# Performance work log

Hardware: AMD Instinct MI355X
Metric: run time of the kernel (lower is better)

Reference implementation:

```python
import jax, jax.numpy as jnp
from jax import lax
import numpy as np
from functools import partial

B, N, T, H, L = 16, 256, 4, 128, 2
VOCAB, OUT_VOCAB, MAX_STEPS = 1000, 1000, 15


def setup_inputs() -> dict:
    key = jax.random.key(0)
    ks = jax.random.split(key, 13)
    data = jax.random.randint(ks[0], (B, N, T), 0, VOCAB)
    true_branch_nodes = jax.random.randint(ks[1], (B, N), 0, N)
    false_branch_nodes = jax.random.randint(ks[2], (B, N), 0, N)
    exit_index = jax.random.randint(ks[3], (B,), 0, N)
    steps = jax.random.randint(ks[4], (B,), 1, MAX_STEPS + 1)
    s_in = 1.0 / np.sqrt(H)
    s_cat = 1.0 / np.sqrt(2 * L * H)
    embed = jax.random.uniform(ks[5], (VOCAB, H), jnp.float32, -0.1, 0.1)
    Wi = jax.random.normal(ks[6], (L, H, 4 * H), jnp.float32) * s_in
    Wh = jax.random.normal(ks[7], (L, H, 4 * H), jnp.float32) * s_in
    b_lstm = jnp.zeros((L, 4 * H), jnp.float32)
    Wb = jax.random.normal(ks[8], (2 * L * H, 2), jnp.float32) * s_cat
    bb = jax.random.normal(ks[9], (2,), jnp.float32) * 1e-6
    Wo = jax.random.normal(ks[10], (2 * L * H, OUT_VOCAB), jnp.float32) * s_cat
    bo = jax.random.normal(ks[11], (OUT_VOCAB,), jnp.float32) * 1e-6
    return dict(data=data, true_branch_nodes=true_branch_nodes,
                false_branch_nodes=false_branch_nodes, exit_index=exit_index,
                steps=steps, embed=embed, Wi=Wi, Wh=Wh, b_lstm=b_lstm,
                Wb=Wb, bb=bb, Wo=Wo, bo=bo)


def _lstm_step(Wi_l, Wh_l, b_l, c, h, x):
    # flax LSTMCell math: gates from input (no bias) + recurrent (bias)
    z = x @ Wi_l + h @ Wh_l + b_l  # [..., 4H]
    i, f, g, o = jnp.split(z, 4, axis=-1)
    c2 = jax.nn.sigmoid(f) * c + jax.nn.sigmoid(i) * jnp.tanh(g)
    h2 = jax.nn.sigmoid(o) * jnp.tanh(c2)
    return c2, h2


def _forward(data, true_branch_nodes, false_branch_nodes, exit_index, steps,
             embed, Wi, Wh, b_lstm, Wb, bb, Wo, bo):
    emb = embed[data]                       # [B, N, T, H]
    cs = jnp.zeros((L, B, N, H), embed.dtype)
    hs = jnp.zeros((L, B, N, H), embed.dtype)
    ip = jnp.zeros((B, N), embed.dtype).at[:, 0].set(1.0)
    b_idx = jnp.arange(B)

    seg_b = jax.vmap(partial(jax.ops.segment_sum, num_segments=N))        # [B,N,...] , [B,N]
    seg_lb = jax.vmap(seg_b, in_axes=(0, None))                           # [L,B,N,H]

    def execute(cs, hs):
        # run the stacked LSTM over the T statement tokens at every node
        def tok_step(carry, x_t):
            cs, hs = carry
            inp = x_t
            nc, nh = [], []
            for l in range(L):
                c2, h2 = _lstm_step(Wi[l], Wh[l], b_lstm[l], cs[l], hs[l], inp)
                nc.append(c2); nh.append(h2)
                inp = h2
            return (jnp.stack(nc), jnp.stack(nh)), None
        (cs, hs), _ = lax.scan(tok_step, (cs, hs), jnp.moveaxis(emb, 2, 0))
        return cs, hs

    def step(carry, _):
        cs, hs, ip, idx = carry
        cs_c, hs_c = execute(cs, hs)
        # exit node keeps its previous hidden state
        cs_c = cs_c.at[:, b_idx, exit_index].set(cs[:, b_idx, exit_index])
        hs_c = hs_c.at[:, b_idx, exit_index].set(hs[:, b_idx, exit_index])
        # branch decision from concatenated (c, h) of every layer: [B, N, 2LH]
        feats = jnp.concatenate([x for l in range(L) for x in (cs_c[l], hs_c[l])], axis=-1)
        branch = jax.nn.softmax(feats @ Wb + bb, axis=-1)
        wt = branch[..., 0] * ip            # [B, N]
        wf = branch[..., 1] * ip
        ip_new = seg_b(wt, true_branch_nodes) + seg_b(wf, false_branch_nodes)
        denom = (ip_new + 1e-7)[None, :, :, None]
        def agg(h):
            return (seg_lb(h * wt[None, :, :, None], true_branch_nodes)
                    + seg_lb(h * wf[None, :, :, None], false_branch_nodes)) / denom
        cs_new, hs_new = agg(cs_c), agg(hs_c)
        live = idx < steps                   # [B]
        cs = jnp.where(live[None, :, None, None], cs_new, cs)
        hs = jnp.where(live[None, :, None, None], hs_new, hs)
        ip = jnp.where(live[:, None], ip_new, ip)
        return (cs, hs, ip, idx + 1), None

    (cs, hs, ip, _), _ = lax.scan(step, (cs, hs, ip, jnp.zeros((), jnp.int32)),
                                  None, length=MAX_STEPS)
    fc = cs[:, b_idx, exit_index]           # [L, B, H]
    fh = hs[:, b_idx, exit_index]
    final = jnp.concatenate([x for l in range(L) for x in (fc[l], fh[l])], axis=-1)
    logits = final @ Wo + bo                # [B, OUT_VOCAB]
    return logits[:, None, :]


def reference(data, true_branch_nodes, false_branch_nodes, exit_index, steps,
              embed, Wi, Wh, b_lstm, Wb, bb, Wo, bo):
    return _forward(data, true_branch_nodes, false_branch_nodes, exit_index,
                    steps, embed, Wi, Wh, b_lstm, Wb, bb, Wo, bo)
```

## Files before the change

### kernel.cpp

```cpp
#include <hip/hip_runtime.h>
#include <hip/hip_bf16.h>
#include <stdint.h>
#include <stddef.h>

static constexpr int BB = 16, NN = 256, TT = 4, HH = 128;
static constexpr int MM = BB * NN;
static constexpr int CC = 512;
static constexpr int OUTV = 1000;
static constexpr int MAXS = 15;
static constexpr int SP = 132;

typedef float f32x4 __attribute__((ext_vector_type(4)));
typedef short s16x8 __attribute__((ext_vector_type(8)));

__device__ __forceinline__ float sigf(float x) { return 1.0f / (1.0f + __expf(-x)); }
__device__ __forceinline__ float tanhr(float x) { return 2.0f / (1.0f + __expf(-2.0f * x)) - 1.0f; }
__device__ __forceinline__ unsigned short f2bu(float a) {
  return __builtin_bit_cast(unsigned short, __float2bfloat16(a));
}
__device__ __forceinline__ unsigned int packh(float a, float b) {
  return (unsigned int)f2bu(a) | ((unsigned int)f2bu(b) << 16);
}
__device__ __forceinline__ float blo(unsigned int u) { return __builtin_bit_cast(float, u << 16); }
__device__ __forceinline__ float bhi(unsigned int u) { return __builtin_bit_cast(float, u & 0xffff0000u); }


__global__ __launch_bounds__(512) void csr_kernel(const int* __restrict__ tb,
                                                  const int* __restrict__ fb,
                                                  int* __restrict__ offs,
                                                  int* __restrict__ edges) {
  const int blk = blockIdx.x;
  const int tid = threadIdx.x;
  __shared__ int cnt[256], sc[256], cur[256];
  if (tid < 256) cnt[tid] = 0;
  __syncthreads();
  const int n = tid >> 1, bit = tid & 1;
  const int tgt = bit ? fb[blk * NN + n] : tb[blk * NN + n];
  atomicAdd(&cnt[tgt], 1);
  __syncthreads();
  if (tid < 256) sc[tid] = cnt[tid];
  __syncthreads();
  for (int ofs = 1; ofs < 256; ofs <<= 1) {
    int t2 = (tid < 256 && tid >= ofs) ? sc[tid - ofs] : 0;
    __syncthreads();
    if (tid < 256) sc[tid] += t2;
    __syncthreads();
  }
  if (tid < 256) { offs[blk * NN + tid] = blk * 2 * NN + sc[tid] - cnt[tid]; cur[tid] = 0; }
  if (blk == 0 && tid == 0) offs[MM] = 2 * MM;
  __syncthreads();
  int lpos = sc[tgt] - cnt[tgt] + atomicAdd(&cur[tgt], 1);
  edges[blk * 2 * NN + lpos] = (n << 1) | bit;
}

__global__ __launch_bounds__(256) void prep_kernel(
    const float* __restrict__ Wh0, const float* __restrict__ Wi1, const float* __restrict__ Wh1,
    const float* __restrict__ embed, const float* __restrict__ Wi0, const float* __restrict__ b0,
    unsigned short* __restrict__ swz, float* __restrict__ tab) {
  const int blk = blockIdx.x;
  const int tid = threadIdx.x;
  if (blk < 768) {
    int i = blk * 256 + tid;
    int mtx = i >> 16, ii = i & 65535;
    const float* W = (mtx == 0) ? Wh0 : (mtx == 1) ? Wi1 : Wh1;
    int j = ii & 7, ln = (ii >> 3) & 63, kb = (ii >> 9) & 3, ct = ii >> 11;
    int n = ln & 15, q = ln >> 4;
    swz[i] = f2bu(W[(kb * 32 + q * 8 + j) * CC + ct * 16 + n]);
    return;
  }
  const int v0 = (blk - 768) * 8;
  __shared__ float A[8][HH];
  for (int s = tid; s < 8 * HH; s += 256) {
    int r = s >> 7, k = s & 127;
    A[r][k] = embed[(size_t)(v0 + r) * HH + k];
  }
  __syncthreads();
  const int j = tid;
  float za[8], zb[8];
  {
    float ba = b0[j], bbv = b0[j + 256];
#pragma unroll
    for (int r = 0; r < 8; ++r) { za[r] = ba; zb[r] = bbv; }
  }
#pragma unroll 4
  for (int k = 0; k < HH; ++k) {
    float wa = Wi0[k * CC + j], wb = Wi0[k * CC + j + 256];
#pragma unroll
    for (int r = 0; r < 8; ++r) { za[r] += A[r][k] * wa; zb[r] += A[r][k] * wb; }
  }
#pragma unroll
  for (int r = 0; r < 8; ++r) {
    tab[(size_t)(v0 + r) * CC + j] = za[r];
    tab[(size_t)(v0 + r) * CC + j + 256] = zb[r];
  }
}


__global__ __launch_bounds__(512) void step_kernel(
    float* __restrict__ Sc0g, float* __restrict__ Sh0g,
    float* __restrict__ Sc1g, float* __restrict__ Sh1g,
    const unsigned int* __restrict__ Pr, unsigned int* __restrict__ Pw,
    const float* __restrict__ wtR, const float* __restrict__ wfR,
    float* __restrict__ wtW, float* __restrict__ wfW,
    const int* __restrict__ offs, const int* __restrict__ edges,
    const float* __restrict__ tab,
    const unsigned short* __restrict__ swzWh0, const unsigned short* __restrict__ swzWi1,
    const unsigned short* __restrict__ swzWh1, const float* __restrict__ b1,
    const float* __restrict__ Wb, const float* __restrict__ bb,
    const int* __restrict__ data, const int* __restrict__ exi,
    const int* __restrict__ steps, int step) {
  const int B = blockIdx.x;
  const int b = (B & 7) | (((B >> 3) & 1) << 3);
  const int g16 = B >> 4;
  const int row0 = b * NN + g16 * 16;
  const int sb = steps[b];
  const bool aggLive = (step >= 1) && ((step - 1) < sb);
  const bool lstmLive = (step < sb);
  if (!aggLive && !lstmLive) return;

  const int tid = threadIdx.x;
  const int w = tid >> 6;
  const int lane = tid & 63;
  const int n16 = lane & 15, qq = lane >> 4;
  const int kcol = w * 16 + n16;
  const int basePos = ((kcol >> 5) * 64 + ((kcol >> 3) & 3) * 16) * 8 + (kcol & 7);

  __shared__ float c0L[16 * SP], h0L[16 * SP], c1L[16 * SP], h1L[16 * SP];
  __shared__ __align__(16) unsigned short hA0[2][2048], hA1[2][2048];
  __shared__ float exitP[512];
  __shared__ float ipL[16];
  __shared__ int toks[64];

  s16x8 B0f[4][4], B1f[4][4];
  float b1v[4];
  const s16x8* pWh0 = (const s16x8*)swzWh0;
  const s16x8* pWh1 = (const s16x8*)swzWh1;
  const s16x8* pWi1 = (const s16x8*)swzWi1;
  if (lstmLive) {
#pragma unroll
    for (int g = 0; g < 4; ++g) {
      int ci = w + 8 * g;
#pragma unroll
      for (int kb = 0; kb < 4; ++kb) {
        B0f[g][kb] = pWh0[(ci * 4 + kb) * 64 + lane];
        B1f[g][kb] = pWh1[(ci * 4 + kb) * 64 + lane];
      }
      b1v[g] = b1[ci * 16 + n16];
    }
    if (tid < 64) toks[tid] = data[(row0 + (tid >> 2)) * TT + (tid & 3)];
  }

  if (aggLive) {
    const int l = tid & 31;
    const int m = tid >> 5;
    const int node = row0 + m;
    const int beg = offs[node], end = offs[node + 1];
    float ac0[4] = {0,0,0,0}, ah0[4] = {0,0,0,0}, ac1[4] = {0,0,0,0}, ah1[4] = {0,0,0,0};
    float wsum = 0.f;
    for (int e = beg; e < end; ++e) {
      int rec = edges[e];
      int src = (b << 8) + (rec >> 1);
      float wv = (rec & 1) ? wfR[src] : wtR[src];
      wsum += wv;
      const uint4* pr = (const uint4*)(Pr + (size_t)src * 256 + 8 * l);
      uint4 u0 = pr[0], u1 = pr[1];
      ac0[0] += wv * blo(u0.x); ac0[1] += wv * bhi(u0.x);
      ac0[2] += wv * blo(u0.y); ac0[3] += wv * bhi(u0.y);
      ah0[0] += wv * blo(u0.z); ah0[1] += wv * bhi(u0.z);
      ah0[2] += wv * blo(u0.w); ah0[3] += wv * bhi(u0.w);
      ac1[0] += wv * blo(u1.x); ac1[1] += wv * bhi(u1.x);
      ac1[2] += wv * blo(u1.y); ac1[3] += wv * bhi(u1.y);
      ah1[0] += wv * blo(u1.z); ah1[1] += wv * bhi(u1.z);
      ah1[2] += wv * blo(u1.w); ah1[3] += wv * bhi(u1.w);
    }
    float inv = 1.0f / (wsum + 1e-7f);
    float4 o0 = { ac0[0]*inv, ac0[1]*inv, ac0[2]*inv, ac0[3]*inv };
    float4 o1 = { ah0[0]*inv, ah0[1]*inv, ah0[2]*inv, ah0[3]*inv };
    float4 o2 = { ac1[0]*inv, ac1[1]*inv, ac1[2]*inv, ac1[3]*inv };
    float4 o3 = { ah1[0]*inv, ah1[1]*inv, ah1[2]*inv, ah1[3]*inv };
    ((float4*)c0L)[m * (SP / 4) + l] = o0;
    ((float4*)h0L)[m * (SP / 4) + l] = o1;
    ((float4*)c1L)[m * (SP / 4) + l] = o2;
    ((float4*)h1L)[m * (SP / 4) + l] = o3;
    if (l == 0) ipL[m] = wsum;
    if (!lstmLive) {
      ((float4*)Sc0g)[node * 32 + l] = o0;
      ((float4*)Sh0g)[node * 32 + l] = o1;
      ((float4*)Sc1g)[node * 32 + l] = o2;
      ((float4*)Sh1g)[node * 32 + l] = o3;
    }
  } else {
    for (int i2 = tid; i2 < 16 * HH; i2 += 512) {
      int m = i2 >> 7, k = i2 & 127;
      c0L[m * SP + k] = 0.f; h0L[m * SP + k] = 0.f;
      c1L[m * SP + k] = 0.f; h1L[m * SP + k] = 0.f;
    }
    if (tid < 16) ipL[tid] = (((row0 + tid) & (NN - 1)) == 0) ? 1.0f : 0.0f;
  }
  if (!lstmLive) return;

  const int exnode = exi[b];
  const int exm = exnode - (g16 * 16);
  __syncthreads();

  if (exm >= 0 && exm < 16 && tid < 128) {
    exitP[tid] = c0L[exm * SP + tid];
    exitP[128 + tid] = h0L[exm * SP + tid];
    exitP[256 + tid] = c1L[exm * SP + tid];
    exitP[384 + tid] = h1L[exm * SP + tid];
  }

  float c0r[4], c1r[4], h0r[4], h1r[4];
#pragma unroll
  for (int r = 0; r < 4; ++r) {
    int m = qq * 4 + r;
    c0r[r] = c0L[m * SP + kcol];
    c1r[r] = c1L[m * SP + kcol];
    h0r[r] = h0L[m * SP + kcol];
    h1r[r] = h1L[m * SP + kcol];
    hA0[0][basePos + m * 8] = f2bu(h0r[r]);
    hA1[0][basePos + m * 8] = f2bu(h1r[r]);
  }
  __syncthreads();

  int cur = 0;
  for (int t = 0; t < TT; ++t) {
    const int nxt = cur ^ 1;
    const s16x8* hA0c = (const s16x8*)hA0[cur];
    const s16x8* hA1c = (const s16x8*)hA1[cur];
    s16x8 a0[4], a1b[4];
#pragma unroll
    for (int kb = 0; kb < 4; ++kb) { a0[kb] = hA0c[kb * 64 + lane]; a1b[kb] = hA1c[kb * 64 + lane]; }
    f32x4 d0[4];
#pragma unroll
    for (int g = 0; g < 4; ++g) {
      int colz = (w + 8 * g) * 16 + n16;
#pragma unroll
      for (int r = 0; r < 4; ++r)
        d0[g][r] = tab[(size_t)toks[(qq * 4 + r) * 4 + t] * CC + colz];
    }

#pragma unroll
    for (int g = 0; g < 4; ++g)
#pragma unroll
      for (int kb = 0; kb < 4; ++kb)
        d0[g] = __builtin_amdgcn_mfma_f32_16x16x32_bf16(a0[kb], B0f[g][kb], d0[g], 0, 0, 0);

#pragma unroll
    for (int r = 0; r < 4; ++r) {
      float cn = sigf(d0[1][r]) * c0r[r] + sigf(d0[0][r]) * tanhr(d0[2][r]);
      float hn = sigf(d0[3][r]) * tanhr(cn);
      c0r[r] = cn; h0r[r] = hn;
      hA0[nxt][basePos + (qq * 4 + r) * 8] = f2bu(hn);
    }
    __syncthreads();

    const s16x8* hA0n = (const s16x8*)hA0[nxt];
    s16x8 a1a[4];
#pragma unroll
    for (int kb = 0; kb < 4; ++kb) a1a[kb] = hA0n[kb * 64 + lane];
    f32x4 d1[4];
#pragma unroll
    for (int g = 0; g < 4; ++g) {
      int ci = w + 8 * g;
      s16x8 wi[4];
#pragma unroll
      for (int kb = 0; kb < 4; ++kb) wi[kb] = pWi1[(ci * 4 + kb) * 64 + lane];
      f32x4 d = { b1v[g], b1v[g], b1v[g], b1v[g] };
#pragma unroll
      for (int kb = 0; kb < 4; ++kb)
        d = __builtin_amdgcn_mfma_f32_16x16x32_bf16(a1a[kb], wi[kb], d, 0, 0, 0);
#pragma unroll
      for (int kb = 0; kb < 4; ++kb)
        d = __builtin_amdgcn_mfma_f32_16x16x32_bf16(a1b[kb], B1f[g][kb], d, 0, 0, 0);
      d1[g] = d;
    }

#pragma unroll
    for (int r = 0; r < 4; ++r) {
      float cn = sigf(d1[1][r]) * c1r[r] + sigf(d1[0][r]) * tanhr(d1[2][r]);
      float hn = sigf(d1[3][r]) * tanhr(cn);
      c1r[r] = cn; h1r[r] = hn;
      hA1[nxt][basePos + (qq * 4 + r) * 8] = f2bu(hn);
    }
    __syncthreads();
    cur = nxt;
  }

#pragma unroll
  for (int r = 0; r < 4; ++r) {
    int m = qq * 4 + r;
    c0L[m * SP + kcol] = c0r[r];
    h0L[m * SP + kcol] = h0r[r];
    c1L[m * SP + kcol] = c1r[r];
    h1L[m * SP + kcol] = h1r[r];
  }
  __syncthreads();

  {
    const int m = tid >> 5, sub = tid & 31;
    const int row = row0 + m;
    const bool isExit = (m == exm);
    float z0 = 0.f, z1 = 0.f;
#pragma unroll
    for (int u = 0; u < 16; ++u) {
      int k = u * 32 + sub;
      int seg = k >> 7, kk = k & 127;
      float fk;
      if (isExit) {
        fk = exitP[seg * 128 + kk];
      } else {
        fk = (seg == 0) ? c0L[m * SP + kk] : (seg == 1) ? h0L[m * SP + kk]
           : (seg == 2) ? c1L[m * SP + kk] : h1L[m * SP + kk];
      }
      z0 += fk * Wb[2 * k];
      z1 += fk * Wb[2 * k + 1];
    }
#pragma unroll
    for (int off = 16; off >= 1; off >>= 1) {
      z0 += __shfl_xor(z0, off);
      z1 += __shfl_xor(z1, off);
    }
    if (sub == 0) {
      z0 += bb[0]; z1 += bb[1];
      float mx = fmaxf(z0, z1);
      float e0 = __expf(z0 - mx), e1 = __expf(z1 - mx);
      float inv = 1.0f / (e0 + e1);
      float ipv = ipL[m];
      wtW[row] = e0 * inv * ipv;
      wfW[row] = e1 * inv * ipv;
    }
  }

  {
    const int m = tid >> 5, l = tid & 31;
    const bool ex = (m == exm);
    const int grow = row0 + m;
    float f0[4], f1[4], f2[4], f3[4];
#pragma unroll
    for (int i = 0; i < 4; ++i) {
      int k = 4 * l + i;
      f0[i] = ex ? exitP[k] : c0L[m * SP + k];
      f1[i] = ex ? exitP[128 + k] : h0L[m * SP + k];
      f2[i] = ex ? exitP[256 + k] : c1L[m * SP + k];
      f3[i] = ex ? exitP[384 + k] : h1L[m * SP + k];
    }
    uint4 o0 = { packh(f0[0], f0[1]), packh(f0[2], f0[3]),
                 packh(f1[0], f1[1]), packh(f1[2], f1[3]) };
    uint4 o1 = { packh(f2[0], f2[1]), packh(f2[2], f2[3]),
                 packh(f3[0], f3[1]), packh(f3[2], f3[3]) };
    uint4* pw = (uint4*)(Pw + (size_t)grow * 256 + 8 * l);
    pw[0] = o0; pw[1] = o1;
  }
}

__global__ void final_kernel(const float* __restrict__ Sc0, const float* __restrict__ Sh0,
                             const float* __restrict__ Sc1, const float* __restrict__ Sh1,
                             const int* __restrict__ exi, const float* __restrict__ Wo,
                             const float* __restrict__ bo, float* __restrict__ out) {
  const int b = blockIdx.x >> 2;
  const int vt = blockIdx.x & 3;
  const int tid = threadIdx.x;
  __shared__ float f[512];
  int row = b * NN + exi[b];
  if (tid < 128) {
    size_t g = (size_t)row * HH + tid;
    f[tid] = Sc0[g];
    f[128 + tid] = Sh0[g];
    f[256 + tid] = Sc1[g];
    f[384 + tid] = Sh1[g];
  }
  __syncthreads();
  if (tid < 250) {
    int v = vt * 250 + tid;
    float acc = bo[v];
#pragma unroll 8
    for (int k = 0; k < 512; ++k) acc += f[k] * Wo[(size_t)k * OUTV + v];
    out[b * OUTV + v] = acc;
  }
}

__global__ void zero_out_kernel(float* __restrict__ out, int n) {
  int i = blockIdx.x * blockDim.x + threadIdx.x;
  if (i < n) out[i] = 0.0f;
}


extern "C" void kernel_launch(void* const* d_in, const int* in_sizes, int n_in,
                              void* d_out, int out_size, void* d_ws, size_t ws_size,
                              hipStream_t stream) {
  const int* data = (const int*)d_in[0];
  const int* tb   = (const int*)d_in[1];
  const int* fb   = (const int*)d_in[2];
  const int* exi  = (const int*)d_in[3];
  const int* steps = (const int*)d_in[4];
  const float* embed = (const float*)d_in[5];
  const float* Wi = (const float*)d_in[6];
  const float* Wh = (const float*)d_in[7];
  const float* bl = (const float*)d_in[8];
  const float* Wb = (const float*)d_in[9];
  const float* bb = (const float*)d_in[10];
  const float* Wo = (const float*)d_in[11];
  const float* bo = (const float*)d_in[12];
  float* out = (float*)d_out;

  const float* Wi0 = Wi;
  const float* Wi1 = Wi + HH * CC;
  const float* Wh0 = Wh;
  const float* Wh1 = Wh + HH * CC;
  const float* b0 = bl;
  const float* b1 = bl + CC;

  float* ws = (float*)d_ws;
  size_t off = 0;
  float* tab = ws + off;  off += (size_t)1024 * CC;
  float* Sc0 = ws + off;  off += (size_t)MM * HH;
  float* Sh0 = ws + off;  off += (size_t)MM * HH;
  float* Sc1 = ws + off;  off += (size_t)MM * HH;
  float* Sh1 = ws + off;  off += (size_t)MM * HH;
  unsigned int* PA = (unsigned int*)(ws + off); off += (size_t)MM * 256;
  unsigned int* PB = (unsigned int*)(ws + off); off += (size_t)MM * 256;
  unsigned short* swz = (unsigned short*)(ws + off); off += 3 * 32768;
  float* wtA = ws + off;  off += MM;
  float* wfA = ws + off;  off += MM;
  float* wtB = ws + off;  off += MM;
  float* wfB = ws + off;  off += MM;
  int* offs  = (int*)(ws + off); off += MM + 16;
  int* edges = (int*)(ws + off); off += 2 * MM;
  (void)in_sizes; (void)n_in; (void)out_size;

  if (ws_size < off * sizeof(float)) {
    zero_out_kernel<<<(BB * OUTV + 255) / 256, 256, 0, stream>>>(out, BB * OUTV);
    return;
  }

  unsigned short* swzWh0 = swz;
  unsigned short* swzWi1 = swz + 65536;
  unsigned short* swzWh1 = swz + 2 * 65536;

  csr_kernel<<<BB, 512, 0, stream>>>(tb, fb, offs, edges);
  prep_kernel<<<893, 256, 0, stream>>>(Wh0, Wi1, Wh1, embed, Wi0, b0, swz, tab);

  for (int s = 0; s <= MAXS; ++s) {
    unsigned int* Pwp = (s & 1) ? PB : PA;
    const unsigned int* Prp = (s & 1) ? PA : PB;
    float* wtWp = (s & 1) ? wtB : wtA;
    float* wfWp = (s & 1) ? wfB : wfA;
    const float* wtRp = (s & 1) ? wtA : wtB;
    const float* wfRp = (s & 1) ? wfA : wfB;
    step_kernel<<<MM / 16, 512, 0, stream>>>(
        Sc0, Sh0, Sc1, Sh1, Prp, Pwp,
        wtRp, wfRp, wtWp, wfWp,
        offs, edges, tab, swzWh0, swzWi1, swzWh1, b1, Wb, bb,
        data, exi, steps, s);
  }
  final_kernel<<<BB * 4, 256, 0, stream>>>(Sc0, Sh0, Sc1, Sh1, exi, Wo, bo, out);
}
```

Before: 551.1 us.

## Fuse setup kernels, fold final projection into step kernel, prefetch next token gates

Merges the CSR build and weight-prep kernels into one launch, with the prep tiles resized to 512 threads. The output projection now runs inside the step kernel: when a batch finishes aggregating, only the block that owns the exit node computes the logits directly, so the four full-state global buffers and the final kernel are removed. The per-token embedding-gate table loads are prefetched one timestep ahead so they overlap the layer-1 MFMA work. Risks are fewer blocks doing the logits (each computes 1000 outputs over 512 inputs), plus extra register pressure from the prefetch buffers.

```diff
diff --git a/kernel.cpp b/kernel.cpp
--- a/kernel.cpp
+++ b/kernel.cpp
@@ -24,43 +24,41 @@
 __device__ __forceinline__ float blo(unsigned int u) { return __builtin_bit_cast(float, u << 16); }
 __device__ __forceinline__ float bhi(unsigned int u) { return __builtin_bit_cast(float, u & 0xffff0000u); }
 
-
-__global__ __launch_bounds__(512) void csr_kernel(const int* __restrict__ tb,
-                                                  const int* __restrict__ fb,
-                                                  int* __restrict__ offs,
-                                                  int* __restrict__ edges) {
-  const int blk = blockIdx.x;
-  const int tid = threadIdx.x;
-  __shared__ int cnt[256], sc[256], cur[256];
-  if (tid < 256) cnt[tid] = 0;
-  __syncthreads();
-  const int n = tid >> 1, bit = tid & 1;
-  const int tgt = bit ? fb[blk * NN + n] : tb[blk * NN + n];
-  atomicAdd(&cnt[tgt], 1);
-  __syncthreads();
-  if (tid < 256) sc[tid] = cnt[tid];
-  __syncthreads();
-  for (int ofs = 1; ofs < 256; ofs <<= 1) {
-    int t2 = (tid < 256 && tid >= ofs) ? sc[tid - ofs] : 0;
-    __syncthreads();
-    if (tid < 256) sc[tid] += t2;
-    __syncthreads();
-  }
-  if (tid < 256) { offs[blk * NN + tid] = blk * 2 * NN + sc[tid] - cnt[tid]; cur[tid] = 0; }
-  if (blk == 0 && tid == 0) offs[MM] = 2 * MM;
-  __syncthreads();
-  int lpos = sc[tgt] - cnt[tgt] + atomicAdd(&cur[tgt], 1);
-  edges[blk * 2 * NN + lpos] = (n << 1) | bit;
-}
-
-__global__ __launch_bounds__(256) void prep_kernel(
+__global__ __launch_bounds__(512) void setup_kernel(
+    const int* __restrict__ tb, const int* __restrict__ fb,
+    int* __restrict__ offs, int* __restrict__ edges,
     const float* __restrict__ Wh0, const float* __restrict__ Wi1, const float* __restrict__ Wh1,
     const float* __restrict__ embed, const float* __restrict__ Wi0, const float* __restrict__ b0,
     unsigned short* __restrict__ swz, float* __restrict__ tab) {
   const int blk = blockIdx.x;
   const int tid = threadIdx.x;
-  if (blk < 768) {
-    int i = blk * 256 + tid;
+  __shared__ int cnt[256], sc[256], cur[256];
+  __shared__ float A[8][HH];
+
+  if (blk < 16) {
+    if (tid < 256) cnt[tid] = 0;
+    __syncthreads();
+    const int n = tid >> 1, bit = tid & 1;
+    const int tgt = bit ? fb[blk * NN + n] : tb[blk * NN + n];
+    atomicAdd(&cnt[tgt], 1);
+    __syncthreads();
+    if (tid < 256) sc[tid] = cnt[tid];
+    __syncthreads();
+    for (int ofs = 1; ofs < 256; ofs <<= 1) {
+      int t2 = (tid < 256 && tid >= ofs) ? sc[tid - ofs] : 0;
+      __syncthreads();
+      if (tid < 256) sc[tid] += t2;
+      __syncthreads();
+    }
+    if (tid < 256) { offs[blk * NN + tid] = blk * 2 * NN + sc[tid] - cnt[tid]; cur[tid] = 0; }
+    if (blk == 0 && tid == 0) offs[MM] = 2 * MM;
+    __syncthreads();
+    int lpos = sc[tgt] - cnt[tgt] + atomicAdd(&cur[tgt], 1);
+    edges[blk * 2 * NN + lpos] = (n << 1) | bit;
+    return;
+  }
+  if (blk < 400) {
+    int i = (blk - 16) * 512 + tid;
     int mtx = i >> 16, ii = i & 65535;
     const float* W = (mtx == 0) ? Wh0 : (mtx == 1) ? Wi1 : Wh1;
     int j = ii & 7, ln = (ii >> 3) & 63, kb = (ii >> 9) & 3, ct = ii >> 11;
@@ -68,37 +66,31 @@
     swz[i] = f2bu(W[(kb * 32 + q * 8 + j) * CC + ct * 16 + n]);
     return;
   }
-  const int v0 = (blk - 768) * 8;
-  __shared__ float A[8][HH];
-  for (int s = tid; s < 8 * HH; s += 256) {
+  const int v0 = (blk - 400) * 8;
+  for (int s = tid; s < 8 * HH; s += 512) {
     int r = s >> 7, k = s & 127;
     A[r][k] = embed[(size_t)(v0 + r) * HH + k];
   }
   __syncthreads();
   const int j = tid;
-  float za[8], zb[8];
+  float za[8];
   {
-    float ba = b0[j], bbv = b0[j + 256];
-#pragma unroll
-    for (int r = 0; r < 8; ++r) { za[r] = ba; zb[r] = bbv; }
+    float ba = b0[j];
+#pragma unroll
+    for (int r = 0; r < 8; ++r) za[r] = ba;
   }
 #pragma unroll 4
   for (int k = 0; k < HH; ++k) {
-    float wa = Wi0[k * CC + j], wb = Wi0[k * CC + j + 256];
-#pragma unroll
-    for (int r = 0; r < 8; ++r) { za[r] += A[r][k] * wa; zb[r] += A[r][k] * wb; }
-  }
-#pragma unroll
-  for (int r = 0; r < 8; ++r) {
-    tab[(size_t)(v0 + r) * CC + j] = za[r];
-    tab[(size_t)(v0 + r) * CC + j + 256] = zb[r];
-  }
+    float wv = Wi0[k * CC + j];
+#pragma unroll
+    for (int r = 0; r < 8; ++r) za[r] += A[r][k] * wv;
+  }
+#pragma unroll
+  for (int r = 0; r < 8; ++r) tab[(size_t)(v0 + r) * CC + j] = za[r];
 }
 
 
 __global__ __launch_bounds__(512) void step_kernel(
-    float* __restrict__ Sc0g, float* __restrict__ Sh0g,
-    float* __restrict__ Sc1g, float* __restrict__ Sh1g,
     const unsigned int* __restrict__ Pr, unsigned int* __restrict__ Pw,
     const float* __restrict__ wtR, const float* __restrict__ wfR,
     float* __restrict__ wtW, float* __restrict__ wfW,
@@ -107,6 +99,7 @@
     const unsigned short* __restrict__ swzWh0, const unsigned short* __restrict__ swzWi1,
     const unsigned short* __restrict__ swzWh1, const float* __restrict__ b1,
     const float* __restrict__ Wb, const float* __restrict__ bb,
+    const float* __restrict__ Wo, const float* __restrict__ bo, float* __restrict__ out,
     const int* __restrict__ data, const int* __restrict__ exi,
     const int* __restrict__ steps, int step) {
   const int B = blockIdx.x;
@@ -117,6 +110,11 @@
   const bool aggLive = (step >= 1) && ((step - 1) < sb);
   const bool lstmLive = (step < sb);
   if (!aggLive && !lstmLive) return;
+
+  const int exnode = exi[b];
+  const int exm = exnode - (g16 * 16);
+  const bool ownExit = (exm >= 0 && exm < 16);
+  if (!lstmLive && !ownExit) return;
 
   const int tid = threadIdx.x;
   const int w = tid >> 6;
@@ -183,12 +181,6 @@
     ((float4*)c1L)[m * (SP / 4) + l] = o2;
     ((float4*)h1L)[m * (SP / 4) + l] = o3;
     if (l == 0) ipL[m] = wsum;
-    if (!lstmLive) {
-      ((float4*)Sc0g)[node * 32 + l] = o0;
-      ((float4*)Sh0g)[node * 32 + l] = o1;
-      ((float4*)Sc1g)[node * 32 + l] = o2;
-      ((float4*)Sh1g)[node * 32 + l] = o3;
-    }
   } else {
     for (int i2 = tid; i2 < 16 * HH; i2 += 512) {
       int m = i2 >> 7, k = i2 & 127;
@@ -197,13 +189,31 @@
     }
     if (tid < 16) ipL[tid] = (((row0 + tid) & (NN - 1)) == 0) ? 1.0f : 0.0f;
   }
-  if (!lstmLive) return;
-
-  const int exnode = exi[b];
-  const int exm = exnode - (g16 * 16);
+
+  if (!lstmLive) {
+    __syncthreads();
+    if (tid < 128) {
+      exitP[tid] = c0L[exm * SP + tid];
+      exitP[128 + tid] = h0L[exm * SP + tid];
+      exitP[256 + tid] = c1L[exm * SP + tid];
+      exitP[384 + tid] = h1L[exm * SP + tid];
+    }
+    __syncthreads();
+#pragma unroll
+    for (int half = 0; half < 2; ++half) {
+      int v = half * 512 + tid;
+      if (v < OUTV) {
+        float acc = bo[v];
+#pragma unroll 8
+        for (int k = 0; k < 512; ++k) acc += exitP[k] * Wo[(size_t)k * OUTV + v];
+        out[b * OUTV + v] = acc;
+      }
+    }
+    return;
+  }
   __syncthreads();
 
-  if (exm >= 0 && exm < 16 && tid < 128) {
+  if (ownExit && tid < 128) {
     exitP[tid] = c0L[exm * SP + tid];
     exitP[128 + tid] = h0L[exm * SP + tid];
     exitP[256 + tid] = c1L[exm * SP + tid];
@@ -221,6 +231,14 @@
     hA0[0][basePos + m * 8] = f2bu(h0r[r]);
     hA1[0][basePos + m * 8] = f2bu(h1r[r]);
   }
+  f32x4 d0c[4];
+#pragma unroll
+  for (int g = 0; g < 4; ++g) {
+    int colz = (w + 8 * g) * 16 + n16;
+#pragma unroll
+    for (int r = 0; r < 4; ++r)
+      d0c[g][r] = tab[(size_t)toks[(qq * 4 + r) * 4 + 0] * CC + colz];
+  }
   __syncthreads();
 
   int cur = 0;
@@ -231,29 +249,32 @@
     s16x8 a0[4], a1b[4];
 #pragma unroll
     for (int kb = 0; kb < 4; ++kb) { a0[kb] = hA0c[kb * 64 + lane]; a1b[kb] = hA1c[kb * 64 + lane]; }
-    f32x4 d0[4];
-#pragma unroll
-    for (int g = 0; g < 4; ++g) {
-      int colz = (w + 8 * g) * 16 + n16;
-#pragma unroll
-      for (int r = 0; r < 4; ++r)
-        d0[g][r] = tab[(size_t)toks[(qq * 4 + r) * 4 + t] * CC + colz];
-    }
 
 #pragma unroll
     for (int g = 0; g < 4; ++g)
 #pragma unroll
       for (int kb = 0; kb < 4; ++kb)
-        d0[g] = __builtin_amdgcn_mfma_f32_16x16x32_bf16(a0[kb], B0f[g][kb], d0[g], 0, 0, 0);
+        d0c[g] = __builtin_amdgcn_mfma_f32_16x16x32_bf16(a0[kb], B0f[g][kb], d0c[g], 0, 0, 0);
 
 #pragma unroll
     for (int r = 0; r < 4; ++r) {
-      float cn = sigf(d0[1][r]) * c0r[r] + sigf(d0[0][r]) * tanhr(d0[2][r]);
-      float hn = sigf(d0[3][r]) * tanhr(cn);
+      float cn = sigf(d0c[1][r]) * c0r[r] + sigf(d0c[0][r]) * tanhr(d0c[2][r]);
+      float hn = sigf(d0c[3][r]) * tanhr(cn);
       c0r[r] = cn; h0r[r] = hn;
       hA0[nxt][basePos + (qq * 4 + r) * 8] = f2bu(hn);
     }
     __syncthreads();
+
+    f32x4 d0n[4];
+    if (t < TT - 1) {
+#pragma unroll
+      for (int g = 0; g < 4; ++g) {
+        int colz = (w + 8 * g) * 16 + n16;
+#pragma unroll
+        for (int r = 0; r < 4; ++r)
+          d0n[g][r] = tab[(size_t)toks[(qq * 4 + r) * 4 + t + 1] * CC + colz];
+      }
+    }
 
     const s16x8* hA0n = (const s16x8*)hA0[nxt];
     s16x8 a1a[4];
@@ -284,6 +305,8 @@
       hA1[nxt][basePos + (qq * 4 + r) * 8] = f2bu(hn);
     }
     __syncthreads();
+#pragma unroll
+    for (int g = 0; g < 4; ++g) d0c[g] = d0n[g];
     cur = nxt;
   }
 
@@ -351,32 +374,6 @@
                  packh(f3[0], f3[1]), packh(f3[2], f3[3]) };
     uint4* pw = (uint4*)(Pw + (size_t)grow * 256 + 8 * l);
     pw[0] = o0; pw[1] = o1;
-  }
-}
-
-__global__ void final_kernel(const float* __restrict__ Sc0, const float* __restrict__ Sh0,
-                             const float* __restrict__ Sc1, const float* __restrict__ Sh1,
-                             const int* __restrict__ exi, const float* __restrict__ Wo,
-                             const float* __restrict__ bo, float* __restrict__ out) {
-  const int b = blockIdx.x >> 2;
-  const int vt = blockIdx.x & 3;
-  const int tid = threadIdx.x;
-  __shared__ float f[512];
-  int row = b * NN + exi[b];
-  if (tid < 128) {
-    size_t g = (size_t)row * HH + tid;
-    f[tid] = Sc0[g];
-    f[128 + tid] = Sh0[g];
-    f[256 + tid] = Sc1[g];
-    f[384 + tid] = Sh1[g];
-  }
-  __syncthreads();
-  if (tid < 250) {
-    int v = vt * 250 + tid;
-    float acc = bo[v];
-#pragma unroll 8
-    for (int k = 0; k < 512; ++k) acc += f[k] * Wo[(size_t)k * OUTV + v];
-    out[b * OUTV + v] = acc;
   }
 }
 
@@ -414,10 +411,6 @@
   float* ws = (float*)d_ws;
   size_t off = 0;
   float* tab = ws + off;  off += (size_t)1024 * CC;
-  float* Sc0 = ws + off;  off += (size_t)MM * HH;
-  float* Sh0 = ws + off;  off += (size_t)MM * HH;
-  float* Sc1 = ws + off;  off += (size_t)MM * HH;
-  float* Sh1 = ws + off;  off += (size_t)MM * HH;
   unsigned int* PA = (unsigned int*)(ws + off); off += (size_t)MM * 256;
   unsigned int* PB = (unsigned int*)(ws + off); off += (size_t)MM * 256;
   unsigned short* swz = (unsigned short*)(ws + off); off += 3 * 32768;
@@ -438,8 +431,8 @@
   unsigned short* swzWi1 = swz + 65536;
   unsigned short* swzWh1 = swz + 2 * 65536;
 
-  csr_kernel<<<BB, 512, 0, stream>>>(tb, fb, offs, edges);
-  prep_kernel<<<893, 256, 0, stream>>>(Wh0, Wi1, Wh1, embed, Wi0, b0, swz, tab);
+  setup_kernel<<<525, 512, 0, stream>>>(tb, fb, offs, edges, Wh0, Wi1, Wh1,
+                                        embed, Wi0, b0, swz, tab);
 
   for (int s = 0; s <= MAXS; ++s) {
     unsigned int* Pwp = (s & 1) ? PB : PA;
@@ -449,10 +442,8 @@
     const float* wtRp = (s & 1) ? wtA : wtB;
     const float* wfRp = (s & 1) ? wfA : wfB;
     step_kernel<<<MM / 16, 512, 0, stream>>>(
-        Sc0, Sh0, Sc1, Sh1, Prp, Pwp,
-        wtRp, wfRp, wtWp, wfWp,
+        Prp, Pwp, wtRp, wfRp, wtWp, wfWp,
         offs, edges, tab, swzWh0, swzWi1, swzWh1, b1, Wb, bb,
-        data, exi, steps, s);
-  }
-  final_kernel<<<BB * 4, 256, 0, stream>>>(Sc0, Sh0, Sc1, Sh1, exi, Wo, bo, out);
-}
+        Wo, bo, out, data, exi, steps, s);
+  }
+}
```

After: 839.0 us. 52.2% more time.
